# Optimization experiments

Hardware: AMD Instinct MI355X
Metric: run time of the kernel (lower is better)

## Reference

```python
import jax, jax.numpy as jnp
import numpy as np

B, T, C = 4, 2048, 1024
H = 16
D = C // H          # 64 head dim
CS = 128            # chunk_size (hard-coded in module)


def setup_inputs() -> dict:
    key = jax.random.key(0)
    ks = jax.random.split(key, 6)
    scale = 0.02
    x = jax.random.normal(ks[0], (B, T, C), dtype=jnp.float32)
    Wq = jax.random.normal(ks[1], (C, C), dtype=jnp.float32) * scale
    Wk = jax.random.normal(ks[2], (C, C), dtype=jnp.float32) * scale
    Wv = jax.random.normal(ks[3], (C, C), dtype=jnp.float32) * scale
    Wo = jax.random.normal(ks[4], (C, C), dtype=jnp.float32) * scale
    alpha_raw = jnp.zeros((1, H, 1, 1), dtype=jnp.float32)
    beta_raw = jnp.zeros((1, H, 1, 1), dtype=jnp.float32)
    return {"x": x, "Wq": Wq, "Wk": Wk, "Wv": Wv, "Wo": Wo,
            "alpha_raw": alpha_raw, "beta_raw": beta_raw}


def reference(x, Wq, Wk, Wv, Wo, alpha_raw, beta_raw):
    Bb, Tt, Cc = x.shape
    nc = Tt // CS
    N = Bb * H * nc  # flattened (batch, head, chunk) recurrence lanes

    # projections -> [B, H, T, D]
    def proj(W):
        return (x @ W).reshape(Bb, Tt, H, D).transpose(0, 2, 1, 3)
    q, k, v = proj(Wq), proj(Wk), proj(Wv)
    # F.normalize(k, dim=-1) with eps=1e-12
    k = k / jnp.maximum(jnp.linalg.norm(k, axis=-1, keepdims=True), 1e-12)

    alpha = jax.nn.sigmoid(alpha_raw).reshape(H) * 0.5  # [H]
    beta = jax.nn.sigmoid(beta_raw).reshape(H) * 0.5    # [H]
    a = jnp.broadcast_to(alpha[None, :, None], (Bb, H, nc)).reshape(N, 1, 1)
    b = jnp.broadcast_to(beta[None, :, None], (Bb, H, nc)).reshape(N, 1, 1)

    # chunk layout [CS, N, D] for time-major scan
    def to_scan(u):
        return u.reshape(Bb, H, nc, CS, D).reshape(N, CS, D).transpose(1, 0, 2)
    qc, kc, vc = to_scan(q), to_scan(k), to_scan(v)

    # --- per-chunk operators: A = prod(I - a k k^T), B accumulates writes ---
    def op_step(carry, kv):
        A, Bo = carry
        kt, vt = kv  # [N, D]
        Ak = jnp.einsum('nij,nj->ni', A, kt)
        A = A - a * (Ak[:, :, None] * kt[:, None, :])
        Bk = jnp.einsum('nij,nj->ni', Bo, kt)
        Bo = Bo - a * (Bk[:, :, None] * kt[:, None, :]) + b * (vt[:, :, None] * kt[:, None, :])
        return (A, Bo), None

    A0 = jnp.broadcast_to(jnp.eye(D, dtype=x.dtype), (N, D, D))
    (Aop, Bop), _ = jax.lax.scan(op_step, (A0, jnp.zeros((N, D, D), x.dtype)), (kc, vc))

    # --- inter-chunk scan: M_{i+1} = M_i A_i + B_i ---
    Aop_c = Aop.reshape(Bb, H, nc, D, D).transpose(2, 0, 1, 3, 4)
    Bop_c = Bop.reshape(Bb, H, nc, D, D).transpose(2, 0, 1, 3, 4)

    def chunk_step(M, ab):
        Ai, Bi = ab
        return jnp.einsum('bhij,bhjk->bhik', M, Ai) + Bi, M

    M_final, M_starts = jax.lax.scan(
        chunk_step, jnp.zeros((Bb, H, D, D), x.dtype), (Aop_c, Bop_c))

    # --- intra-chunk application: y_t = M_t q_t; rank-1 delta update ---
    M0 = M_starts.transpose(1, 2, 0, 3, 4).reshape(N, D, D)

    def proc_step(M, qkv):
        qt, kt, vt = qkv
        yt = jnp.einsum('nij,nj->ni', M, qt)  # == q_t @ M^T (inference path)
        Mk = jnp.einsum('nij,nj->ni', M, kt)
        M = M - a * (Mk[:, :, None] * kt[:, None, :]) + b * (vt[:, :, None] * kt[:, None, :])
        return M, yt

    _, ys = jax.lax.scan(proc_step, M0, (qc, kc, vc))  # [CS, N, D]
    y = ys.transpose(1, 0, 2).reshape(Bb, H, Tt, D)
    y = y.transpose(0, 2, 1, 3).reshape(Bb, Tt, Cc)
    y = y @ Wo  # c_proj (dropout=0 -> identity)
    return (y, M_final)
```

## Files before the change

kernel.cpp:

```cpp
#include <hip/hip_runtime.h>
#include <stdint.h>


#define DEV __device__ __forceinline__

typedef __attribute__((ext_vector_type(4))) float f32x4;
typedef __attribute__((ext_vector_type(8))) __bf16 bf16x8;
typedef __attribute__((ext_vector_type(4))) __bf16 bf16x4;

typedef const __attribute__((address_space(1))) uint32_t* gas1_t;
typedef __attribute__((address_space(3))) uint32_t* las3_t;

DEV void gload_lds16(const void* g, void* l) {
  __builtin_amdgcn_global_load_lds((gas1_t)g, (las3_t)l, 16, 0, 0);
}

DEV float sgm(float x) { return 1.f / (1.f + __expf(-x)); }

template <int CTRL>
DEV float dpp_mov(float x) {
  return __builtin_bit_cast(
      float, __builtin_amdgcn_mov_dpp(__builtin_bit_cast(int, x), CTRL, 0xF, 0xF, true));
}
DEV float row16_reduce(float x) {
  x += dpp_mov<0x121>(x);
  x += dpp_mov<0x122>(x);
  x += dpp_mov<0x124>(x);
  x += dpp_mov<0x128>(x);
  return x;
}

DEV int swzb(int row, int col, int stride) {
  return ((row * stride + col) << 1) ^ ((row & 7) << 4);
}
DEV bf16x8 ldfrag(const __bf16* B, int row, int col, int stride) {
  return *(const bf16x8*)((const char*)B + swzb(row, col, stride));
}
DEV __bf16 ldsc(const __bf16* B, int row, int col, int stride) {
  return *(const __bf16*)((const char*)B + swzb(row, col, stride));
}
DEV void stb(__bf16* B, int row, int col, int stride, __bf16 v) {
  *(__bf16*)((char*)B + swzb(row, col, stride)) = v;
}
DEV void stb4(__bf16* B, int row, int c4, int stride, bf16x4 v) {
  *(bf16x4*)((char*)B + swzb(row, c4, stride)) = v;
}
DEV int goffn(int tr) {
  int m = tr >> 1;
  return (tr & 1) ? (2 * m * m + 4 * m + 2) : (2 * m * m + 2 * m);
}
DEV int stile(int tr, int sc) { return ((tr * (tr + 1)) / 2 + sc) * 256; }

__global__ __launch_bounds__(256) void cast_f32_bf16(const float* __restrict__ in,
                                                     __bf16* __restrict__ out) {
  int idx = blockIdx.x * 256 + threadIdx.x;
  float4 v = ((const float4*)in)[idx];
  bf16x4 o;
  o[0] = (__bf16)v.x; o[1] = (__bf16)v.y; o[2] = (__bf16)v.z; o[3] = (__bf16)v.w;
  ((bf16x4*)out)[idx] = o;
}

__global__ __launch_bounds__(256) void transpose_cast(const float* __restrict__ W,
                                                      __bf16* __restrict__ Wt) {
  __shared__ float tile[32][33];
  int tx = threadIdx.x & 31, ty = threadIdx.x >> 5;
  int n0 = blockIdx.x * 32, k0 = blockIdx.y * 32;
#pragma unroll
  for (int u = 0; u < 4; ++u)
    tile[ty + u * 8][tx] = W[(size_t)(k0 + ty + u * 8) * 1024 + n0 + tx];
  __syncthreads();
#pragma unroll
  for (int u = 0; u < 4; ++u)
    Wt[(size_t)(n0 + ty + u * 8) * 1024 + k0 + tx] = (__bf16)tile[tx][ty + u * 8];
}

__global__ __launch_bounds__(256) void gemm_bt(const __bf16* __restrict__ A,
                                               const __bf16* __restrict__ Bt,
                                               float* __restrict__ Cf,
                                               __bf16* __restrict__ Cb, int mode) {
  const int t = threadIdx.x;
  const int wv = t >> 6, lane = t & 63;
  const int bm = blockIdx.y, bn = blockIdx.x;
  const int K = 1024;
  __shared__ __bf16 lA[4096];
  __shared__ __bf16 lB[4096];
  f32x4 acc[4][4];
#pragma unroll
  for (int m = 0; m < 4; ++m)
#pragma unroll
    for (int n = 0; n < 4; ++n) acc[m][n] = 0.f;
  const int wr = wv >> 1, wc = wv & 1;
  const int fr = lane & 15, fk = (lane >> 4) * 8;
  const int e0 = (wv * 128 + lane) * 8;
  const int e1 = (wv * 128 + 64 + lane) * 8;
  const int r0s = e0 >> 5, c0s = e0 & 31;
  const int r1s = e1 >> 5, c1s = e1 & 31;
  for (int k0 = 0; k0 < K; k0 += 32) {
    gload_lds16(A + (size_t)(bm * 128 + r0s) * K + k0 + c0s, lA + wv * 1024);
    gload_lds16(Bt + (size_t)(bn * 128 + r0s) * K + k0 + c0s, lB + wv * 1024);
    gload_lds16(A + (size_t)(bm * 128 + r1s) * K + k0 + c1s, lA + wv * 1024 + 512);
    gload_lds16(Bt + (size_t)(bn * 128 + r1s) * K + k0 + c1s, lB + wv * 1024 + 512);
    __syncthreads();
    bf16x8 af[4], bg[4];
#pragma unroll
    for (int m = 0; m < 4; ++m)
      af[m] = *(const bf16x8*)(lA + (wr * 64 + m * 16 + fr) * 32 + fk);
#pragma unroll
    for (int n = 0; n < 4; ++n)
      bg[n] = *(const bf16x8*)(lB + (wc * 64 + n * 16 + fr) * 32 + fk);
#pragma unroll
    for (int m = 0; m < 4; ++m)
#pragma unroll
      for (int n = 0; n < 4; ++n)
        acc[m][n] = __builtin_amdgcn_mfma_f32_16x16x32_bf16(af[m], bg[n], acc[m][n], 0, 0, 0);
    __syncthreads();
  }
  const int rr = (lane >> 4) * 4, cl = lane & 15;
#pragma unroll
  for (int m = 0; m < 4; ++m) {
#pragma unroll
    for (int n = 0; n < 4; ++n) {
#pragma unroll
      for (int rg = 0; rg < 4; ++rg) {
        int row = bm * 128 + wr * 64 + m * 16 + rr + rg;
        int col = bn * 128 + wc * 64 + n * 16 + cl;
        float val = acc[m][n][rg];
        if (mode == 0) {
          Cf[(size_t)row * 1024 + col] = val;
        } else {
          int b = row >> 11, tk = row & 2047;
          int h = col >> 6, d = col & 63;
          Cb[(((size_t)b * 16 + h) * 2048 + tk) * 64 + d] = (__bf16)val;
        }
      }
    }
  }
}

__global__ __launch_bounds__(512, 6) void wy_ab(const __bf16* __restrict__ kb,
                                                const __bf16* __restrict__ vb,
                                                const float* __restrict__ ar,
                                                const float* __restrict__ br,
                                                __bf16* __restrict__ Ug,
                                                __bf16* __restrict__ Wgb,
                                                __bf16* __restrict__ ATg,
                                                float* __restrict__ Bop) {
  int n = blockIdx.x, h = (n >> 4) & 15;
  float a = sgm(ar[h]) * 0.5f;
  float b = sgm(br[h]) * 0.5f;
  int t = threadIdx.x, wid = t >> 6, lane = t & 63;
  int fr = lane & 15, fkq = lane >> 4, fk = fkq * 8;
  __shared__ __attribute__((aligned(16))) char pool[51200];
  __bf16* Ks  = (__bf16*)pool;
  __bf16* MTu = (__bf16*)pool;
  __bf16* MTw = (__bf16*)(pool + 16384);
  __bf16* Sng = (__bf16*)(pool + 32768);
  __bf16* KT  = (__bf16*)(pool + 32768);
  const __bf16* kg = kb + (size_t)n * 8192;
  const __bf16* vg = vb + (size_t)n * 8192;
  bf16x8 zz;
#pragma unroll
  for (int e = 0; e < 8; ++e) zz[e] = (__bf16)0.f;
  f32x4 c0 = {0.f, 0.f, 0.f, 0.f};
  bf16x4 kreg[4];
#pragma unroll
  for (int it = 0; it < 4; ++it) {
    int u = it * 512 + t;
    int row = u >> 4, c4 = (u & 15) * 4;
    bf16x4 kh = ((const bf16x4*)kg)[u];
    float kf[4];
#pragma unroll
    for (int e = 0; e < 4; ++e) kf[e] = (float)kh[e];
    float ssq = kf[0] * kf[0] + kf[1] * kf[1] + kf[2] * kf[2] + kf[3] * kf[3];
    ssq = row16_reduce(ssq);
    float inv = 1.f / fmaxf(sqrtf(ssq), 1e-12f);
    bf16x4 kn;
#pragma unroll
    for (int e = 0; e < 4; ++e) kn[e] = (__bf16)(kf[e] * inv);
    kreg[it] = kn;
    stb4(Ks, row, c4, 64, kn);
  }
  __syncthreads();
  for (int p = wid; p < 36; p += 8) {
    int tr = 0, pp = p;
    while (pp > tr) { pp -= (tr + 1); ++tr; }
    int sc = pp;
    f32x4 acc = {0.f, 0.f, 0.f, 0.f};
#pragma unroll
    for (int ks = 0; ks < 2; ++ks)
      acc = __builtin_amdgcn_mfma_f32_16x16x32_bf16(
          ldfrag(Ks, tr * 16 + fr, ks * 32 + fk, 64),
          ldfrag(Ks, sc * 16 + fr, ks * 32 + fk, 64), acc, 0, 0, 0);
    __bf16* dst = Sng + stile(tr, sc);
#pragma unroll
    for (int rg = 0; rg < 4; ++rg) {
      int r = fkq * 4 + rg;
      float v = -a * acc[rg];
      if (tr == sc && fr >= r) v = 0.f;
      dst[r * 16 + fr] = (__bf16)v;
    }
  }
  f32x4 U[4], W[4];
#pragma unroll
  for (int ct = 0; ct < 4; ++ct) {
#pragma unroll
    for (int rg = 0; rg < 4; ++rg) {
      int row = wid * 16 + fkq * 4 + rg, col = ct * 16 + fr;
      U[ct][rg] = (float)ldsc(Ks, row, col, 64);
      W[ct][rg] = b * (float)vg[row * 64 + col];
    }
  }
  __syncthreads();
  {
    __bf16* scr  = ((__bf16*)pool) + wid * 2048;
    __bf16* tNT  = scr;
    __bf16* tN2R = scr + 256;
    __bf16* tN2T = scr + 512;
    __bf16* tN4R = scr + 768;
    __bf16* tN4T = scr + 1024;
    __bf16* tN8T = scr + 1280;
    __bf16* tPR  = scr + 1536;
    __bf16* Nd = Sng + stile(wid, wid);
    float nv[4];
#pragma unroll
    for (int rg = 0; rg < 4; ++rg) {
      nv[rg] = (float)Nd[(fkq * 4 + rg) * 16 + fr];
      tNT[fr * 16 + fkq * 4 + rg] = (__bf16)nv[rg];
    }
    asm volatile("s_waitcnt lgkmcnt(0)" ::: "memory");
    bf16x8 af = (fk < 16) ? *(const bf16x8*)(Nd + fr * 16 + fk) : zz;
    bf16x8 bop = (fk < 16) ? *(const bf16x8*)(tNT + fr * 16 + fk) : zz;
    f32x4 X = __builtin_amdgcn_mfma_f32_16x16x32_bf16(af, bop, c0, 0, 0, 0);
#pragma unroll
    for (int rg = 0; rg < 4; ++rg) {
      __bf16 v = (__bf16)X[rg];
      tN2R[(fkq * 4 + rg) * 16 + fr] = v;
      tN2T[fr * 16 + fkq * 4 + rg] = v;
    }
    asm volatile("s_waitcnt lgkmcnt(0)" ::: "memory");
    af = (fk < 16) ? *(const bf16x8*)(tN2R + fr * 16 + fk) : zz;
    bop = (fk < 16) ? *(const bf16x8*)(tN2T + fr * 16 + fk) : zz;
    X = __builtin_amdgcn_mfma_f32_16x16x32_bf16(af, bop, c0, 0, 0, 0);
#pragma unroll
    for (int rg = 0; rg < 4; ++rg) {
      __bf16 v = (__bf16)X[rg];
      tN4R[(fkq * 4 + rg) * 16 + fr] = v;
      tN4T[fr * 16 + fkq * 4 + rg] = v;
    }
    asm volatile("s_waitcnt lgkmcnt(0)" ::: "memory");
    af = (fk < 16) ? *(const bf16x8*)(tN4R + fr * 16 + fk) : zz;
    bop = (fk < 16) ? *(const bf16x8*)(tN4T + fr * 16 + fk) : zz;
    X = __builtin_amdgcn_mfma_f32_16x16x32_bf16(af, bop, c0, 0, 0, 0);
#pragma unroll
    for (int rg = 0; rg < 4; ++rg)
      tN8T[fr * 16 + fkq * 4 + rg] = (__bf16)X[rg];
    f32x4 P;
#pragma unroll
    for (int rg = 0; rg < 4; ++rg)
      P[rg] = ((fkq * 4 + rg) == fr ? 1.f : 0.f) + nv[rg];
#pragma unroll
    for (int d = 0; d < 3; ++d) {
      const __bf16* tB = (d == 0) ? tN2T : (d == 1) ? tN4T : tN8T;
#pragma unroll
      for (int rg = 0; rg < 4; ++rg)
        tPR[(fkq * 4 + rg) * 16 + fr] = (__bf16)P[rg];
      asm volatile("s_waitcnt lgkmcnt(0)" ::: "memory");
      af = (fk < 16) ? *(const bf16x8*)(tPR + fr * 16 + fk) : zz;
      bop = (fk < 16) ? *(const bf16x8*)(tB + fr * 16 + fk) : zz;
      P = __builtin_amdgcn_mfma_f32_16x16x32_bf16(af, bop, P, 0, 0, 0);
    }
#pragma unroll
    for (int rg = 0; rg < 4; ++rg)
      Nd[(fkq * 4 + rg) * 16 + fr] = (__bf16)P[rg];
  }
  __syncthreads();
  for (int bb = 0; bb < 8; ++bb) {
    if (wid == bb) {
#pragma unroll
      for (int ct = 0; ct < 4; ++ct) {
        bf16x4 uu, ww;
#pragma unroll
        for (int rg = 0; rg < 4; ++rg) {
          uu[rg] = (__bf16)U[ct][rg];
          ww[rg] = (__bf16)W[ct][rg];
        }
        stb4(MTu, ct * 16 + fr, bb * 16 + fkq * 4, 128, uu);
        stb4(MTw, ct * 16 + fr, bb * 16 + fkq * 4, 128, ww);
      }
      asm volatile("s_waitcnt lgkmcnt(0)" ::: "memory");
      const __bf16* invT = Sng + stile(bb, bb);
      bf16x8 afv = (fk < 16) ? *(const bf16x8*)(invT + fr * 16 + fk) : zz;
#pragma unroll
      for (int ct = 0; ct < 4; ++ct) {
        bf16x8 bu = (fk < 16) ? ldfrag(MTu, ct * 16 + fr, bb * 16 + fk, 128) : zz;
        bf16x8 bw = (fk < 16) ? ldfrag(MTw, ct * 16 + fr, bb * 16 + fk, 128) : zz;
        U[ct] = __builtin_amdgcn_mfma_f32_16x16x32_bf16(afv, bu, c0, 0, 0, 0);
        W[ct] = __builtin_amdgcn_mfma_f32_16x16x32_bf16(afv, bw, c0, 0, 0, 0);
      }
#pragma unroll
      for (int ct = 0; ct < 4; ++ct) {
        bf16x4 uu, ww;
#pragma unroll
        for (int rg = 0; rg < 4; ++rg) {
          uu[rg] = (__bf16)U[ct][rg];
          ww[rg] = (__bf16)W[ct][rg];
        }
        stb4(MTu, ct * 16 + fr, bb * 16 + fkq * 4, 128, uu);
        stb4(MTw, ct * 16 + fr, bb * 16 + fkq * 4, 128, ww);
      }
    }
    __syncthreads();
    if (wid > bb) {
      bf16x8 af = zz;
      if (fk < 16) af = *(const bf16x8*)(Sng + stile(wid, bb) + fr * 16 + fk);
#pragma unroll
      for (int ct = 0; ct < 4; ++ct) {
        bf16x8 bu = zz, bw = zz;
        if (fk < 16) {
          bu = ldfrag(MTu, ct * 16 + fr, bb * 16 + fk, 128);
          bw = ldfrag(MTw, ct * 16 + fr, bb * 16 + fk, 128);
        }
        U[ct] = __builtin_amdgcn_mfma_f32_16x16x32_bf16(af, bu, U[ct], 0, 0, 0);
        W[ct] = __builtin_amdgcn_mfma_f32_16x16x32_bf16(af, bw, W[ct], 0, 0, 0);
      }
    }
  }
#pragma unroll
  for (int it = 0; it < 4; ++it) {
    int u = it * 512 + t;
    int row = u >> 4, c4 = (u & 15) * 4;
#pragma unroll
    for (int e = 0; e < 4; ++e) stb(KT, c4 + e, row, 128, kreg[it][e]);
  }
  __bf16* ugo = Ug + (size_t)n * 8192;
  __bf16* wgo = Wgb + (size_t)n * 8192;
#pragma unroll
  for (int ct = 0; ct < 4; ++ct)
#pragma unroll
    for (int rg = 0; rg < 4; ++rg) {
      int row = wid * 16 + fkq * 4 + rg, col = ct * 16 + fr;
      ugo[row * 64 + col] = (__bf16)U[ct][rg];
      wgo[row * 64 + col] = (__bf16)W[ct][rg];
    }
  __syncthreads();
#pragma unroll
  for (int q = 0; q < 4; ++q) {
    int tile = wid + q * 8;
    int mat = tile >> 4;
    int ti = (tile >> 2) & 3, tj = tile & 3;
    f32x4 acc = {0.f, 0.f, 0.f, 0.f};
    if (mat == 0) {
#pragma unroll
      for (int ks = 0; ks < 4; ++ks)
        acc = __builtin_amdgcn_mfma_f32_16x16x32_bf16(
            ldfrag(KT, ti * 16 + fr, ks * 32 + fk, 128),
            ldfrag(MTu, tj * 16 + fr, ks * 32 + fk, 128), acc, 0, 0, 0);
      char* dst = (char*)(ATg + (size_t)n * 4096);
#pragma unroll
      for (int rg = 0; rg < 4; ++rg) {
        int i = ti * 16 + fkq * 4 + rg, j = tj * 16 + fr;
        float v = (i == j ? 1.f : 0.f) - a * acc[rg];
        *(__bf16*)(dst + swzb(i, j, 64)) = (__bf16)v;
      }
    } else {
#pragma unroll
      for (int ks = 0; ks < 4; ++ks)
        acc = __builtin_amdgcn_mfma_f32_16x16x32_bf16(
            ldfrag(MTw, ti * 16 + fr, ks * 32 + fk, 128),
            ldfrag(KT, tj * 16 + fr, ks * 32 + fk, 128), acc, 0, 0, 0);
      float* dst = Bop + (size_t)n * 4096;
#pragma unroll
      for (int rg = 0; rg < 4; ++rg)
        dst[(ti * 16 + fkq * 4 + rg) * 64 + tj * 16 + fr] = acc[rg];
    }
  }
}

__global__ __launch_bounds__(512) void chunk_scan(const __bf16* __restrict__ ATg,
                                                  const float* __restrict__ Bop,
                                                  __bf16* __restrict__ Mst,
                                                  float* __restrict__ Mfinal) {
  int bh = blockIdx.x;
  int t = threadIdx.x, wid = t >> 6, lane = t & 63;
  int fr = lane & 15, fkq = lane >> 4, fk = fkq * 8;
  int ti = wid & 3, tj0 = (wid >> 2) << 1;
  __shared__ __bf16 Mh[4096];
  __shared__ __bf16 Ml[4096];
  __shared__ __bf16 At[2][4096];
  f32x4 acc[2];
  acc[0] = 0.f;
  acc[1] = 0.f;
  gload_lds16(ATg + (size_t)bh * 16 * 4096 + t * 8, At[0] + t * 8);
  for (int c = 0; c < 16; ++c) {
    int cur = c & 1;
    if (c < 15)
      gload_lds16(ATg + ((size_t)(bh * 16 + c + 1)) * 4096 + t * 8,
                  At[cur ^ 1] + t * 8);
    __bf16* mstc = Mst + ((size_t)(bh * 16 + c)) * 4096;
#pragma unroll
    for (int p = 0; p < 2; ++p) {
      int tj = tj0 + p;
#pragma unroll
      for (int rg = 0; rg < 4; ++rg) {
        int row = ti * 16 + fkq * 4 + rg, col = tj * 16 + fr;
        float v = acc[p][rg];
        __bf16 hi = (__bf16)v;
        mstc[row * 64 + col] = hi;
        stb(Mh, row, col, 64, hi);
        stb(Ml, row, col, 64, (__bf16)(v - (float)hi));
      }
    }
    __syncthreads();
    size_t bb = ((size_t)(bh * 16 + c)) * 4096;
#pragma unroll
    for (int p = 0; p < 2; ++p) {
      int tj = tj0 + p;
      f32x4 na;
#pragma unroll
      for (int rg = 0; rg < 4; ++rg)
        na[rg] = Bop[bb + (ti * 16 + fkq * 4 + rg) * 64 + tj * 16 + fr];
#pragma unroll
      for (int ks = 0; ks < 2; ++ks) {
        bf16x8 bfrag = ldfrag(At[cur], tj * 16 + fr, ks * 32 + fk, 64);
        bf16x8 ah = ldfrag(Mh, ti * 16 + fr, ks * 32 + fk, 64);
        bf16x8 al = ldfrag(Ml, ti * 16 + fr, ks * 32 + fk, 64);
        na = __builtin_amdgcn_mfma_f32_16x16x32_bf16(ah, bfrag, na, 0, 0, 0);
        na = __builtin_amdgcn_mfma_f32_16x16x32_bf16(al, bfrag, na, 0, 0, 0);
      }
      acc[p] = na;
    }
    __syncthreads();
  }
#pragma unroll
  for (int p = 0; p < 2; ++p) {
    int tj = tj0 + p;
#pragma unroll
    for (int rg = 0; rg < 4; ++rg)
      Mfinal[(size_t)bh * 4096 + (ti * 16 + fkq * 4 + rg) * 64 + tj * 16 + fr] =
          acc[p][rg];
  }
}

__global__ __launch_bounds__(512, 4) void y_assemble(const __bf16* __restrict__ qb,
                                                     const __bf16* __restrict__ kb,
                                                     const __bf16* __restrict__ Ug,
                                                     const __bf16* __restrict__ Wgb,
                                                     const __bf16* __restrict__ Mst,
                                                     const float* __restrict__ ar,
                                                     __bf16* __restrict__ ybf) {
  int n = blockIdx.x, h = (n >> 4) & 15, b = n >> 8, c = n & 15;
  float a = sgm(ar[h]) * 0.5f;
  int t = threadIdx.x, wid = t >> 6, lane = t & 63;
  int fr = lane & 15, fk = (lane >> 4) * 8;
  __shared__ __bf16 Qs[8192];
  __shared__ __bf16 Rs[8192];
  __shared__ __bf16 M0s[4096];
  __shared__ __bf16 Gs[10240];
  __shared__ __bf16 WtT[8192];
  const __bf16* qg = qb + (size_t)n * 8192;
  const __bf16* kg = kb + (size_t)n * 8192;
  const __bf16* mg = Mst + (size_t)n * 4096;
#pragma unroll
  for (int it = 0; it < 4; ++it) {
    int u = it * 512 + t;
    int row = u >> 4, c4 = (u & 15) * 4;
    stb4(Qs, row, c4, 64, ((const bf16x4*)qg)[u]);
    bf16x4 kh = ((const bf16x4*)kg)[u];
    float kf[4];
#pragma unroll
    for (int e = 0; e < 4; ++e) kf[e] = (float)kh[e];
    float ssq = kf[0] * kf[0] + kf[1] * kf[1] + kf[2] * kf[2] + kf[3] * kf[3];
    ssq = row16_reduce(ssq);
    float inv = 1.f / fmaxf(sqrtf(ssq), 1e-12f);
    bf16x4 kn;
#pragma unroll
    for (int e = 0; e < 4; ++e) kn[e] = (__bf16)(kf[e] * inv);
    stb4(Rs, row, c4, 64, kn);
  }
#pragma unroll
  for (int it = 0; it < 2; ++it) {
    int u = it * 512 + t;
    int row = u >> 4, c4 = (u & 15) * 4;
    stb4(M0s, row, c4, 64, ((const bf16x4*)mg)[u]);
  }
#pragma unroll
  for (int pz = 0; pz < 2; ++pz) {
    int e = pz * 512 + t;
    int m = e >> 8, idx = e & 255;
    Gs[(2 * m * m + 4 * m + 1) * 256 + idx] = (__bf16)0.f;
  }
  __syncthreads();
  for (int p = wid; p < 36; p += 8) {
    int tr = 0, pp = p;
    while (pp > tr) { pp -= (tr + 1); ++tr; }
    int sc = pp;
    f32x4 acc = {0.f, 0.f, 0.f, 0.f};
#pragma unroll
    for (int ks = 0; ks < 2; ++ks)
      acc = __builtin_amdgcn_mfma_f32_16x16x32_bf16(
          ldfrag(Qs, tr * 16 + fr, ks * 32 + fk, 64),
          ldfrag(Rs, sc * 16 + fr, ks * 32 + fk, 64), acc, 0, 0, 0);
    int row0 = (lane >> 4) * 4, col = lane & 15;
    __bf16* gt = Gs + (goffn(tr) + sc) * 256;
#pragma unroll
    for (int rg = 0; rg < 4; ++rg) {
      int r = row0 + rg;
      float v = acc[rg];
      if (tr == sc && col >= r) v = 0.f;
      gt[r * 16 + col] = (__bf16)v;
    }
  }
  __syncthreads();
  const __bf16* ug = Ug + (size_t)n * 8192;
  const __bf16* wg = Wgb + (size_t)n * 8192;
#pragma unroll
  for (int it = 0; it < 4; ++it) {
    int u = it * 512 + t;
    int row = u >> 4, c4 = (u & 15) * 4;
    stb4(Rs, row, c4, 64, ((const bf16x4*)ug)[u]);
  }
  __syncthreads();
#pragma unroll
  for (int q = 0; q < 4; ++q) {
    int tile = wid + q * 8;
    int ti = tile >> 2, tj = tile & 3;
    f32x4 acc = {0.f, 0.f, 0.f, 0.f};
#pragma unroll
    for (int ks = 0; ks < 2; ++ks)
      acc = __builtin_amdgcn_mfma_f32_16x16x32_bf16(
          ldfrag(Rs, ti * 16 + fr, ks * 32 + fk, 64),
          ldfrag(M0s, tj * 16 + fr, ks * 32 + fk, 64), acc, 0, 0, 0);
    int row0 = (lane >> 4) * 4, col = lane & 15;
#pragma unroll
    for (int rg = 0; rg < 4; ++rg) {
      int s = ti * 16 + row0 + rg, i = tj * 16 + col;
      float wv = (float)wg[s * 64 + i];
      stb(WtT, i, s, 128, (__bf16)(wv - a * acc[rg]));
    }
  }
  __syncthreads();
  __bf16* yg = ybf + ((size_t)(b * 2048 + c * 128)) * 1024 + h * 64;
#pragma unroll
  for (int q = 0; q < 4; ++q) {
    int tile = wid + q * 8;
    int ti = tile >> 2, tj = tile & 3;
    f32x4 acc = {0.f, 0.f, 0.f, 0.f};
#pragma unroll
    for (int ks = 0; ks < 2; ++ks)
      acc = __builtin_amdgcn_mfma_f32_16x16x32_bf16(
          ldfrag(Qs, ti * 16 + fr, ks * 32 + fk, 64),
          ldfrag(M0s, tj * 16 + fr, ks * 32 + fk, 64), acc, 0, 0, 0);
    int goffv = goffn(ti);
    int np = (ti + 2) >> 1;
    for (int ks = 0; ks < np; ++ks) {
      int gtile = goffv + ks * 2 + (fk >> 4);
      bf16x8 af = *(const bf16x8*)(Gs + gtile * 256 + fr * 16 + (fk & 15));
      acc = __builtin_amdgcn_mfma_f32_16x16x32_bf16(
          af, ldfrag(WtT, tj * 16 + fr, ks * 32 + fk, 128), acc, 0, 0, 0);
    }
    int row0 = (lane >> 4) * 4, col = lane & 15;
#pragma unroll
    for (int rg = 0; rg < 4; ++rg) {
      int tt = ti * 16 + row0 + rg, d = tj * 16 + col;
      yg[(size_t)tt * 1024 + d] = (__bf16)acc[rg];
    }
  }
}

extern "C" void kernel_launch(void* const* d_in, const int* in_sizes, int n_in,
                              void* d_out, int out_size, void* d_ws, size_t ws_size,
                              hipStream_t stream) {
  const float* x  = (const float*)d_in[0];
  const float* Wq = (const float*)d_in[1];
  const float* Wk = (const float*)d_in[2];
  const float* Wv = (const float*)d_in[3];
  const float* Wo = (const float*)d_in[4];
  const float* ar = (const float*)d_in[5];
  const float* br = (const float*)d_in[6];

  char* ws = (char*)d_ws;
  __bf16* xb  = (__bf16*)ws;
  __bf16* ybf = xb;
  __bf16* wqt = (__bf16*)(ws + (17u << 20));
  __bf16* wkt = wqt + (1u << 20);
  __bf16* wvt = wkt + (1u << 20);
  __bf16* wot = wvt + (1u << 20);
  __bf16* qb  = (__bf16*)(ws + (25u << 20));
  __bf16* kb  = (__bf16*)(ws + (42u << 20));
  __bf16* vb  = (__bf16*)(ws + (59u << 20));
  __bf16* Ugb = (__bf16*)(ws + (76u << 20));
  __bf16* Wgb = (__bf16*)(ws + (93u << 20));
  __bf16* ATg = (__bf16*)(ws + (110u << 20));
  float* Bop  = (float*)(ws + (127u << 20));
  __bf16* Mst = (__bf16*)(ws + (144u << 20));

  float* yout = (float*)d_out;
  float* Mfin = yout + 8388608;

  cast_f32_bf16<<<8192, 256, 0, stream>>>(x, xb);
  dim3 tg(32, 32);
  transpose_cast<<<tg, 256, 0, stream>>>(Wq, wqt);
  transpose_cast<<<tg, 256, 0, stream>>>(Wk, wkt);
  transpose_cast<<<tg, 256, 0, stream>>>(Wv, wvt);
  transpose_cast<<<tg, 256, 0, stream>>>(Wo, wot);

  dim3 gg(8, 64);
  gemm_bt<<<gg, 256, 0, stream>>>(xb, wqt, nullptr, qb, 1);
  gemm_bt<<<gg, 256, 0, stream>>>(xb, wkt, nullptr, kb, 1);
  gemm_bt<<<gg, 256, 0, stream>>>(xb, wvt, nullptr, vb, 1);

  wy_ab<<<1024, 512, 0, stream>>>(kb, vb, ar, br, Ugb, Wgb, ATg, Bop);
  chunk_scan<<<64, 512, 0, stream>>>(ATg, Bop, Mst, Mfin);
  y_assemble<<<1024, 512, 0, stream>>>(qb, kb, Ugb, Wgb, Mst, ar, ybf);

  gemm_bt<<<gg, 256, 0, stream>>>(ybf, wot, yout, nullptr, 0);
}
```

Measured before the change: 223.3 us.

## Fuse Q/K/V projections into one GEMM and store Bop in bf16

Concatenates the transposed Wq/Wk/Wv weights into one buffer and launches a single GEMM over a 24-wide column grid. The epilogue routes each column block to the q, k or v output buffer. This cuts two kernel launches and fills the GPU better. Separately, the per-chunk B operator is written and read as bf16 instead of fp32, halving that traffic at some precision cost in the inter-chunk scan.

```diff
diff --git a/kernel.cpp b/kernel.cpp
--- a/kernel.cpp
+++ b/kernel.cpp
@@ -128,9 +128,11 @@
         if (mode == 0) {
           Cf[(size_t)row * 1024 + col] = val;
         } else {
+          int buf = col >> 10, cc = col & 1023;
           int b = row >> 11, tk = row & 2047;
-          int h = col >> 6, d = col & 63;
-          Cb[(((size_t)b * 16 + h) * 2048 + tk) * 64 + d] = (__bf16)val;
+          int h = cc >> 6, d = cc & 63;
+          Cb[(size_t)buf * 8388608 + (((size_t)b * 16 + h) * 2048 + tk) * 64 + d] =
+              (__bf16)val;
         }
       }
     }
@@ -144,7 +146,7 @@
                                                 __bf16* __restrict__ Ug,
                                                 __bf16* __restrict__ Wgb,
                                                 __bf16* __restrict__ ATg,
-                                                float* __restrict__ Bop) {
+                                                __bf16* __restrict__ Bop) {
   int n = blockIdx.x, h = (n >> 4) & 15;
   float a = sgm(ar[h]) * 0.5f;
   float b = sgm(br[h]) * 0.5f;
@@ -368,16 +370,16 @@
         acc = __builtin_amdgcn_mfma_f32_16x16x32_bf16(
             ldfrag(MTw, ti * 16 + fr, ks * 32 + fk, 128),
             ldfrag(KT, tj * 16 + fr, ks * 32 + fk, 128), acc, 0, 0, 0);
-      float* dst = Bop + (size_t)n * 4096;
+      __bf16* dst = Bop + (size_t)n * 4096;
 #pragma unroll
       for (int rg = 0; rg < 4; ++rg)
-        dst[(ti * 16 + fkq * 4 + rg) * 64 + tj * 16 + fr] = acc[rg];
+        dst[(ti * 16 + fkq * 4 + rg) * 64 + tj * 16 + fr] = (__bf16)acc[rg];
     }
   }
 }
 
 __global__ __launch_bounds__(512) void chunk_scan(const __bf16* __restrict__ ATg,
-                                                  const float* __restrict__ Bop,
+                                                  const __bf16* __restrict__ Bop,
                                                   __bf16* __restrict__ Mst,
                                                   float* __restrict__ Mfinal) {
   int bh = blockIdx.x;
@@ -418,7 +420,7 @@
       f32x4 na;
 #pragma unroll
       for (int rg = 0; rg < 4; ++rg)
-        na[rg] = Bop[bb + (ti * 16 + fkq * 4 + rg) * 64 + tj * 16 + fr];
+        na[rg] = (float)Bop[bb + (ti * 16 + fkq * 4 + rg) * 64 + tj * 16 + fr];
 #pragma unroll
       for (int ks = 0; ks < 2; ++ks) {
         bf16x8 bfrag = ldfrag(At[cur], tj * 16 + fr, ks * 32 + fk, 64);
@@ -579,39 +581,36 @@
   const float* br = (const float*)d_in[6];
 
   char* ws = (char*)d_ws;
-  __bf16* xb  = (__bf16*)ws;
-  __bf16* ybf = xb;
-  __bf16* wqt = (__bf16*)(ws + (17u << 20));
-  __bf16* wkt = wqt + (1u << 20);
-  __bf16* wvt = wkt + (1u << 20);
-  __bf16* wot = wvt + (1u << 20);
-  __bf16* qb  = (__bf16*)(ws + (25u << 20));
-  __bf16* kb  = (__bf16*)(ws + (42u << 20));
-  __bf16* vb  = (__bf16*)(ws + (59u << 20));
-  __bf16* Ugb = (__bf16*)(ws + (76u << 20));
-  __bf16* Wgb = (__bf16*)(ws + (93u << 20));
-  __bf16* ATg = (__bf16*)(ws + (110u << 20));
-  float* Bop  = (float*)(ws + (127u << 20));
-  __bf16* Mst = (__bf16*)(ws + (144u << 20));
+  __bf16* xb    = (__bf16*)ws;
+  __bf16* ybf   = xb;
+  __bf16* wqkvt = (__bf16*)(ws + (17u << 20));
+  __bf16* wot   = (__bf16*)(ws + (23u << 20));
+  __bf16* qb    = (__bf16*)(ws + (25u << 20));
+  __bf16* kb    = qb + 8388608;
+  __bf16* vb    = kb + 8388608;
+  __bf16* Ugb   = (__bf16*)(ws + (76u << 20));
+  __bf16* Wgb   = (__bf16*)(ws + (93u << 20));
+  __bf16* ATg   = (__bf16*)(ws + (110u << 20));
+  __bf16* Bop   = (__bf16*)(ws + (127u << 20));
+  __bf16* Mst   = (__bf16*)(ws + (144u << 20));
 
   float* yout = (float*)d_out;
   float* Mfin = yout + 8388608;
 
   cast_f32_bf16<<<8192, 256, 0, stream>>>(x, xb);
   dim3 tg(32, 32);
-  transpose_cast<<<tg, 256, 0, stream>>>(Wq, wqt);
-  transpose_cast<<<tg, 256, 0, stream>>>(Wk, wkt);
-  transpose_cast<<<tg, 256, 0, stream>>>(Wv, wvt);
+  transpose_cast<<<tg, 256, 0, stream>>>(Wq, wqkvt);
+  transpose_cast<<<tg, 256, 0, stream>>>(Wk, wqkvt + (1u << 20));
+  transpose_cast<<<tg, 256, 0, stream>>>(Wv, wqkvt + (2u << 20));
   transpose_cast<<<tg, 256, 0, stream>>>(Wo, wot);
 
-  dim3 gg(8, 64);
-  gemm_bt<<<gg, 256, 0, stream>>>(xb, wqt, nullptr, qb, 1);
-  gemm_bt<<<gg, 256, 0, stream>>>(xb, wkt, nullptr, kb, 1);
-  gemm_bt<<<gg, 256, 0, stream>>>(xb, wvt, nullptr, vb, 1);
+  dim3 gqkv(24, 64);
+  gemm_bt<<<gqkv, 256, 0, stream>>>(xb, wqkvt, nullptr, qb, 1);
 
   wy_ab<<<1024, 512, 0, stream>>>(kb, vb, ar, br, Ugb, Wgb, ATg, Bop);
   chunk_scan<<<64, 512, 0, stream>>>(ATg, Bop, Mst, Mfin);
   y_assemble<<<1024, 512, 0, stream>>>(qb, kb, Ugb, Wgb, Mst, ar, ybf);
 
-  gemm_bt<<<gg, 256, 0, stream>>>(ybf, wot, yout, nullptr, 0);
-}
+  dim3 go(8, 64);
+  gemm_bt<<<go, 256, 0, stream>>>(ybf, wot, yout, nullptr, 0);
+}
```

After: 212.9 us. 4.6% less time.
